# Kernel tuning notes

Hardware: AMD Instinct MI355X
Metric: run time of the kernel (lower is better)

Reference implementation:

```python
import jax, jax.numpy as jnp
import numpy as np

N, E, D, HID, OUT, R = 100000, 640000, 128, 128, 128, 8


def setup_inputs() -> dict:
    key = jax.random.key(0)
    ks = jax.random.split(key, 12)
    x = jax.random.normal(ks[0], (N, D), dtype=jnp.float32)
    src = jax.random.randint(ks[1], (E,), 0, N)
    dst = jax.random.randint(ks[2], (E,), 0, N)
    etype = jax.random.randint(ks[3], (E,), 0, R)
    s = 0.05
    W_rel = jax.random.normal(ks[4], (R, D, OUT), dtype=jnp.float32) * s
    loop_w = jax.random.normal(ks[5], (D, OUT), dtype=jnp.float32) * s
    rel_bias = jax.random.normal(ks[6], (OUT,), dtype=jnp.float32) * s
    W1 = jax.random.normal(ks[7], (D + HID, 2 * HID), dtype=jnp.float32) * s
    b1 = jax.random.normal(ks[8], (2 * HID,), dtype=jnp.float32) * s
    W2 = jax.random.normal(ks[9], (D + 2 * HID, OUT), dtype=jnp.float32) * s
    b2 = jax.random.normal(ks[10], (OUT,), dtype=jnp.float32) * s
    return {"x": x, "src": src, "dst": dst, "etype": etype,
            "W_rel": W_rel, "loop_w": loop_w, "rel_bias": rel_bias,
            "W1": W1, "b1": b1, "W2": W2, "b2": b2}


def reference(x, src, dst, etype, W_rel, loop_w, rel_bias, W1, b1, W2, b2):
    n = x.shape[0]
    # RelGraphConv (low_mem): transform all nodes once per relation, then
    # gather the (relation, src)-specific message per edge.  [R, N, OUT]
    h_rel = jnp.einsum('nd,rdo->rno', x, W_rel)
    m = h_rel[etype, src]                                   # [E, OUT]
    agg = jax.ops.segment_sum(m, dst, num_segments=n)       # sum at dst
    msg = agg + x @ loop_w + rel_bias                       # self-loop + bias
    # concat-MLP update (is_block=False -> dst_x = x), activation = tanh
    mid = jnp.tanh(jnp.concatenate([x, msg], axis=1) @ W1 + b1)
    return jnp.concatenate([x, mid], axis=1) @ W2 + b2
```

## Files before the change

### kernel.cpp

```cpp
#include <hip/hip_runtime.h>

#define NN 100000
#define NE 640000
#define RR 8
#define NBIN 800000

typedef unsigned short u16;
typedef u16 u16x4 __attribute__((ext_vector_type(4)));
typedef u16 u16x8 __attribute__((ext_vector_type(8)));
typedef __bf16 bf16x8 __attribute__((ext_vector_type(8)));
typedef float f32x4 __attribute__((ext_vector_type(4)));

#define OFF_MSG     0u
#define OFF_MIDB    51200000u
#define OFF_XB      102400000u
#define OFF_WT      128000000u
#define OFF_W1T     128296960u
#define OFF_W2T     128428032u
#define OFF_BUCKET  128527360u
#define OFF_CSROFF  131088384u
#define OFF_CUR     134289408u
#define OFF_PSUM    137490432u

__device__ inline u16 f2bf(float f) {
  unsigned u = __float_as_uint(f);
  u += 0x7FFF + ((u >> 16) & 1);
  return (u16)(u >> 16);
}
__device__ inline float bf2f(u16 h) { return __uint_as_float(((unsigned)h) << 16); }

__global__ void k_cvt_x(const float* __restrict__ x, u16* __restrict__ xb) {
  const int i = (blockIdx.x * 256 + threadIdx.x) * 4;
  const float4 v = *(const float4*)(x + i);
  u16x4 o;
  o.x = f2bf(v.x); o.y = f2bf(v.y); o.z = f2bf(v.z); o.w = f2bf(v.w);
  *(u16x4*)(xb + i) = o;
}

__global__ void k_cvt_wrel(const float* __restrict__ W, const float* __restrict__ Lw,
                           u16* __restrict__ Wt) {
  const int idx = blockIdx.x * 256 + threadIdx.x;
  const int r = idx >> 14, o = (idx >> 7) & 127, d = idx & 127;
  Wt[idx] = f2bf(r < 8 ? W[(r << 14) + (d << 7) + o] : Lw[(d << 7) + o]);
}

__global__ void k_cvt_w1(const float* __restrict__ W1, u16* __restrict__ W1t) {
  const int idx = blockIdx.x * 256 + threadIdx.x;
  const int o = idx >> 8, i = idx & 255;
  W1t[idx] = f2bf(W1[i * 256 + o]);
}

__global__ void k_cvt_w2(const float* __restrict__ W2, u16* __restrict__ W2t) {
  const int idx = blockIdx.x * 256 + threadIdx.x;
  const int o = idx / 384, i = idx % 384;
  W2t[idx] = f2bf(W2[i * 128 + o]);
}

__global__ void k_hist(const int* __restrict__ dst, const int* __restrict__ et,
                       int* __restrict__ cnt) {
  const int e = blockIdx.x * 256 + threadIdx.x;
  if (e < NE) atomicAdd(&cnt[dst[e] * 8 + et[e]], 1);
}

__global__ void k_scanA(const int* __restrict__ cnt, int* __restrict__ psum) {
  __shared__ int sc[256];
  const int tid = threadIdx.x, base = blockIdx.x * 1024 + tid * 4;
  int s = 0;
#pragma unroll
  for (int t = 0; t < 4; ++t) { const int i = base + t; if (i < NBIN) s += cnt[i]; }
  sc[tid] = s; __syncthreads();
  for (int d = 128; d > 0; d >>= 1) {
    if (tid < d) sc[tid] += sc[tid + d];
    __syncthreads();
  }
  if (tid == 0) psum[blockIdx.x] = sc[0];
}

__global__ void k_scanB(int* __restrict__ psum) {
  __shared__ int sc[1024];
  const int tid = threadIdx.x;
  const int v = (tid < 782) ? psum[tid] : 0;
  sc[tid] = v; __syncthreads();
  for (int d = 1; d < 1024; d <<= 1) {
    const int t = (tid >= d) ? sc[tid - d] : 0;
    __syncthreads();
    sc[tid] += t;
    __syncthreads();
  }
  if (tid < 782) psum[tid] = sc[tid] - v;
}

__global__ void k_scanC(int* __restrict__ cnt , const int* __restrict__ psum,
                        int* __restrict__ off) {
  __shared__ int sc[256];
  const int tid = threadIdx.x, base = blockIdx.x * 1024 + tid * 4;
  int c[4], s = 0;
#pragma unroll
  for (int t = 0; t < 4; ++t) {
    const int i = base + t;
    c[t] = (i < NBIN) ? cnt[i] : 0;
    s += c[t];
  }
  sc[tid] = s; __syncthreads();
  for (int d = 1; d < 256; d <<= 1) {
    const int t = (tid >= d) ? sc[tid - d] : 0;
    __syncthreads();
    sc[tid] += t;
    __syncthreads();
  }
  int run = psum[blockIdx.x] + sc[tid] - s;
#pragma unroll
  for (int t = 0; t < 4; ++t) {
    const int i = base + t;
    if (i < NBIN) { off[i] = run; cnt[i] = run; run += c[t]; }
  }
  if (blockIdx.x == 0 && tid == 0) off[NBIN] = NE;
}

__global__ void k_scatter(const int* __restrict__ src, const int* __restrict__ dst,
                          const int* __restrict__ et, int* __restrict__ cur,
                          int* __restrict__ bucket) {
  const int e = blockIdx.x * 256 + threadIdx.x;
  if (e < NE) {
    const int pos = atomicAdd(&cur[dst[e] * 8 + et[e]], 1);
    bucket[pos] = src[e];
  }
}

#define ATS 136
__global__ __launch_bounds__(256) void k_edge_msg(
    const u16* __restrict__ xb, const u16* __restrict__ Wt,
    const int* __restrict__ csroff, const int* __restrict__ bucket,
    const float* __restrict__ rel_bias, float* __restrict__ msg) {
  __shared__ u16 At[32 * ATS];
  __shared__ int soff[257];
  const int tid = threadIdx.x;
  const int v0 = blockIdx.x * 32;

  soff[tid] = csroff[v0 * 8 + tid];
  if (tid == 0) soff[256] = csroff[v0 * 8 + 256];

  const int wave = tid >> 6, lane = tid & 63;
  const int l16 = lane & 15, quad = lane >> 4;
  const int rt = wave & 1, cb = (wave >> 1) << 6;
  const int si = tid >> 3, sj = tid & 7;
  __syncthreads();

  f32x4 acc[4] = {};

  for (int r = 0; r < 9; ++r) {
    float a[16] = {};
    int pbeg, pend;
    if (r < 8) { pbeg = soff[si * 8 + r]; pend = soff[si * 8 + r + 1]; }
    else       { pbeg = 0; pend = 1; }
    for (int p = pbeg; p < pend; ++p) {
      const int s = (r < 8) ? bucket[p] : (v0 + si);
      const u16* xp = xb + ((size_t)s << 7) + sj * 16;
      const u16x8 h0 = *(const u16x8*)(xp);
      const u16x8 h1 = *(const u16x8*)(xp + 8);
#pragma unroll
      for (int t = 0; t < 8; ++t) { a[t] += bf2f(h0[t]); a[8 + t] += bf2f(h1[t]); }
    }
    u16x8 o0, o1;
#pragma unroll
    for (int t = 0; t < 8; ++t) { o0[t] = f2bf(a[t]); o1[t] = f2bf(a[8 + t]); }
    *(u16x8*)&At[si * ATS + sj * 16]     = o0;
    *(u16x8*)&At[si * ATS + sj * 16 + 8] = o1;
    __syncthreads();

    bf16x8 afr[4];
#pragma unroll
    for (int t = 0; t < 4; ++t)
      afr[t] = *(const bf16x8*)&At[(rt * 16 + l16) * ATS + quad * 8 + t * 32];
    const u16* wb = Wt + (r << 14);
#pragma unroll
    for (int c = 0; c < 4; ++c) {
      const u16* wp = wb + (size_t)(cb + c * 16 + l16) * 128 + quad * 8;
#pragma unroll
      for (int t = 0; t < 4; ++t)
        acc[c] = __builtin_amdgcn_mfma_f32_16x16x32_bf16(afr[t], *(const bf16x8*)(wp + t * 32), acc[c], 0, 0, 0);
    }
    __syncthreads();
  }

#pragma unroll
  for (int c = 0; c < 4; ++c) {
    const int col = cb + c * 16 + l16;
    const float bias = rel_bias[col];
#pragma unroll
    for (int reg = 0; reg < 4; ++reg) {
      const int row = v0 + rt * 16 + quad * 4 + reg;
      msg[(size_t)row * 128 + col] = acc[c][reg] + bias;
    }
  }
}

#define A1S 264
__global__ __launch_bounds__(256) void k_mlp1(
    const u16* __restrict__ xb, const float* __restrict__ msg,
    const u16* __restrict__ W1t, const float* __restrict__ b1,
    u16* __restrict__ midb) {
  __shared__ u16 At[32 * A1S];
  const int tid = threadIdx.x;
  const int v0 = blockIdx.x * 32;
  const int si = tid >> 3, sj = tid & 7;

  {
    const u16* xp = xb + ((size_t)(v0 + si) << 7) + sj * 16;
    *(u16x8*)&At[si * A1S + sj * 16]     = *(const u16x8*)(xp);
    *(u16x8*)&At[si * A1S + sj * 16 + 8] = *(const u16x8*)(xp + 8);
  }
  {
    const float* mp = msg + (size_t)(v0 + si) * 128 + sj * 16;
    u16x8 o0, o1;
#pragma unroll
    for (int t = 0; t < 8; ++t) { o0[t] = f2bf(mp[t]); o1[t] = f2bf(mp[8 + t]); }
    *(u16x8*)&At[si * A1S + 128 + sj * 16]     = o0;
    *(u16x8*)&At[si * A1S + 128 + sj * 16 + 8] = o1;
  }
  __syncthreads();

  const int wave = tid >> 6, lane = tid & 63;
  const int l16 = lane & 15, quad = lane >> 4;
  const int rt = wave & 1, ch = (wave >> 1) << 7;

  f32x4 acc[8] = {};
  for (int kt = 0; kt < 8; ++kt) {
    const bf16x8 af = *(const bf16x8*)&At[(rt * 16 + l16) * A1S + kt * 32 + quad * 8];
#pragma unroll
    for (int ct = 0; ct < 8; ++ct) {
      const u16* wp = W1t + (size_t)(ch + ct * 16 + l16) * 256 + kt * 32 + quad * 8;
      acc[ct] = __builtin_amdgcn_mfma_f32_16x16x32_bf16(af, *(const bf16x8*)(wp), acc[ct], 0, 0, 0);
    }
  }

#pragma unroll
  for (int ct = 0; ct < 8; ++ct) {
    const int col = ch + ct * 16 + l16;
    const float bias = b1[col];
#pragma unroll
    for (int reg = 0; reg < 4; ++reg) {
      const int row = v0 + rt * 16 + quad * 4 + reg;
      midb[(size_t)row * 256 + col] = f2bf(tanhf(acc[ct][reg] + bias));
    }
  }
}

#define A2S 392
__global__ __launch_bounds__(256) void k_mlp2(
    const u16* __restrict__ xb, const u16* __restrict__ midb,
    const u16* __restrict__ W2t, const float* __restrict__ b2,
    float* __restrict__ out) {
  __shared__ u16 At[32 * A2S];
  const int tid = threadIdx.x;
  const int v0 = blockIdx.x * 32;
  const int si = tid >> 3, sj = tid & 7;

  {
    const u16* xp = xb + ((size_t)(v0 + si) << 7) + sj * 16;
    *(u16x8*)&At[si * A2S + sj * 16]     = *(const u16x8*)(xp);
    *(u16x8*)&At[si * A2S + sj * 16 + 8] = *(const u16x8*)(xp + 8);
  }
  {
    const u16* mp = midb + ((size_t)(v0 + si) << 8) + sj * 32;
#pragma unroll
    for (int t = 0; t < 4; ++t)
      *(u16x8*)&At[si * A2S + 128 + sj * 32 + t * 8] = *(const u16x8*)(mp + t * 8);
  }
  __syncthreads();

  const int wave = tid >> 6, lane = tid & 63;
  const int l16 = lane & 15, quad = lane >> 4;
  const int rt = wave & 1, cb = (wave >> 1) << 6;

  f32x4 acc[4] = {};
  for (int kt = 0; kt < 12; ++kt) {
    const bf16x8 af = *(const bf16x8*)&At[(rt * 16 + l16) * A2S + kt * 32 + quad * 8];
#pragma unroll
    for (int ct = 0; ct < 4; ++ct) {
      const u16* wp = W2t + (size_t)(cb + ct * 16 + l16) * 384 + kt * 32 + quad * 8;
      acc[ct] = __builtin_amdgcn_mfma_f32_16x16x32_bf16(af, *(const bf16x8*)(wp), acc[ct], 0, 0, 0);
    }
  }

#pragma unroll
  for (int ct = 0; ct < 4; ++ct) {
    const int col = cb + ct * 16 + l16;
    const float bias = b2[col];
#pragma unroll
    for (int reg = 0; reg < 4; ++reg) {
      const int row = v0 + rt * 16 + quad * 4 + reg;
      out[(size_t)row * 128 + col] = acc[ct][reg] + bias;
    }
  }
}

extern "C" void kernel_launch(void* const* d_in, const int* in_sizes, int n_in,
                              void* d_out, int out_size, void* d_ws, size_t ws_size,
                              hipStream_t stream) {
  (void)in_sizes; (void)n_in; (void)out_size; (void)ws_size;
  const float* x        = (const float*)d_in[0];
  const int*   src      = (const int*)d_in[1];
  const int*   dst      = (const int*)d_in[2];
  const int*   et       = (const int*)d_in[3];
  const float* W_rel    = (const float*)d_in[4];
  const float* loop_w   = (const float*)d_in[5];
  const float* rel_bias = (const float*)d_in[6];
  const float* W1       = (const float*)d_in[7];
  const float* b1       = (const float*)d_in[8];
  const float* W2       = (const float*)d_in[9];
  const float* b2       = (const float*)d_in[10];
  float* out = (float*)d_out;

  char* ws = (char*)d_ws;
  float* msg    = (float*)(ws + OFF_MSG);
  u16*   midb   = (u16*)(ws + OFF_MIDB);
  u16*   xb     = (u16*)(ws + OFF_XB);
  u16*   Wt     = (u16*)(ws + OFF_WT);
  u16*   W1t    = (u16*)(ws + OFF_W1T);
  u16*   W2t    = (u16*)(ws + OFF_W2T);
  int*   bucket = (int*)(ws + OFF_BUCKET);
  int*   csroff = (int*)(ws + OFF_CSROFF);
  int*   cur    = (int*)(ws + OFF_CUR);
  int*   psum   = (int*)(ws + OFF_PSUM);

  hipMemsetAsync(cur, 0, (size_t)NBIN * 4, stream);

  k_cvt_x   <<<(NN * 128) / 1024, 256, 0, stream>>>(x, xb);
  k_cvt_wrel<<<(9 * 16384) / 256, 256, 0, stream>>>(W_rel, loop_w, Wt);
  k_cvt_w1  <<<(256 * 256) / 256, 256, 0, stream>>>(W1, W1t);
  k_cvt_w2  <<<(128 * 384) / 256, 256, 0, stream>>>(W2, W2t);

  k_hist    <<<(NE + 255) / 256, 256, 0, stream>>>(dst, et, cur);
  k_scanA   <<<782, 256, 0, stream>>>(cur, psum);
  k_scanB   <<<1, 1024, 0, stream>>>(psum);
  k_scanC   <<<782, 256, 0, stream>>>(cur, psum, csroff);
  k_scatter <<<(NE + 255) / 256, 256, 0, stream>>>(src, dst, et, cur, bucket);

  k_edge_msg<<<NN / 32, 256, 0, stream>>>(xb, Wt, csroff, bucket, rel_bias, msg);
  k_mlp1    <<<NN / 32, 256, 0, stream>>>(xb, msg, W1t, b1, midb);
  k_mlp2    <<<NN / 32, 256, 0, stream>>>(xb, midb, W2t, b2, out);
}
```

Baseline: 638.7 us.

## Rebalance edge aggregation with flat edge-parallel LDS atomics over relation-grouped bins

```diff
diff --git a/kernel.cpp b/kernel.cpp
--- a/kernel.cpp
+++ b/kernel.cpp
@@ -29,6 +29,10 @@
 }
 __device__ inline float bf2f(u16 h) { return __uint_as_float(((unsigned)h) << 16); }
 
+__device__ inline int edge_bin(int d, int r) {
+  return (((d >> 5) * 2 + (r >> 2)) << 7) + ((d & 31) << 2) + (r & 3);
+}
+
 __global__ void k_cvt_x(const float* __restrict__ x, u16* __restrict__ xb) {
   const int i = (blockIdx.x * 256 + threadIdx.x) * 4;
   const float4 v = *(const float4*)(x + i);
@@ -59,7 +63,7 @@
 __global__ void k_hist(const int* __restrict__ dst, const int* __restrict__ et,
                        int* __restrict__ cnt) {
   const int e = blockIdx.x * 256 + threadIdx.x;
-  if (e < NE) atomicAdd(&cnt[dst[e] * 8 + et[e]], 1);
+  if (e < NE) atomicAdd(&cnt[edge_bin(dst[e], et[e])], 1);
 }
 
 __global__ void k_scanA(const int* __restrict__ cnt, int* __restrict__ psum) {
@@ -119,66 +123,93 @@
 
 __global__ void k_scatter(const int* __restrict__ src, const int* __restrict__ dst,
                           const int* __restrict__ et, int* __restrict__ cur,
-                          int* __restrict__ bucket) {
+                          unsigned* __restrict__ bucket) {
   const int e = blockIdx.x * 256 + threadIdx.x;
   if (e < NE) {
-    const int pos = atomicAdd(&cur[dst[e] * 8 + et[e]], 1);
-    bucket[pos] = src[e];
-  }
-}
-
-#define ATS 136
+    const int d = dst[e], r = et[e];
+    const int pos = atomicAdd(&cur[edge_bin(d, r)], 1);
+    bucket[pos] = (unsigned)src[e] | ((unsigned)(d & 31) << 17) | ((unsigned)(r & 3) << 22);
+  }
+}
+
+#define ACCS 132
 __global__ __launch_bounds__(256) void k_edge_msg(
     const u16* __restrict__ xb, const u16* __restrict__ Wt,
-    const int* __restrict__ csroff, const int* __restrict__ bucket,
+    const int* __restrict__ csroff, const unsigned* __restrict__ bucket,
     const float* __restrict__ rel_bias, float* __restrict__ msg) {
-  __shared__ u16 At[32 * ATS];
-  __shared__ int soff[257];
+  __shared__ float accF[4 * 32 * ACCS];
   const int tid = threadIdx.x;
   const int v0 = blockIdx.x * 32;
-
-  soff[tid] = csroff[v0 * 8 + tid];
-  if (tid == 0) soff[256] = csroff[v0 * 8 + 256];
-
   const int wave = tid >> 6, lane = tid & 63;
   const int l16 = lane & 15, quad = lane >> 4;
   const int rt = wave & 1, cb = (wave >> 1) << 6;
-  const int si = tid >> 3, sj = tid & 7;
-  __syncthreads();
+
+  const int base0 = csroff[blockIdx.x * 256];
+  const int base1 = csroff[blockIdx.x * 256 + 128];
+  const int base2 = csroff[blockIdx.x * 256 + 256];
 
   f32x4 acc[4] = {};
 
-  for (int r = 0; r < 9; ++r) {
-    float a[16] = {};
-    int pbeg, pend;
-    if (r < 8) { pbeg = soff[si * 8 + r]; pend = soff[si * 8 + r + 1]; }
-    else       { pbeg = 0; pend = 1; }
-    for (int p = pbeg; p < pend; ++p) {
-      const int s = (r < 8) ? bucket[p] : (v0 + si);
-      const u16* xp = xb + ((size_t)s << 7) + sj * 16;
+  {
+    const u16* xp = xb + ((size_t)(v0 + rt * 16 + l16) << 7) + quad * 8;
+    bf16x8 afr[4];
+#pragma unroll
+    for (int t = 0; t < 4; ++t) afr[t] = *(const bf16x8*)(xp + t * 32);
+    const u16* wb = Wt + (8 << 14);
+#pragma unroll
+    for (int c = 0; c < 4; ++c) {
+      const u16* wp = wb + (size_t)(cb + c * 16 + l16) * 128 + quad * 8;
+#pragma unroll
+      for (int t = 0; t < 4; ++t)
+        acc[c] = __builtin_amdgcn_mfma_f32_16x16x32_bf16(afr[t], *(const bf16x8*)(wp + t * 32), acc[c], 0, 0, 0);
+    }
+  }
+
+#pragma unroll
+  for (int ph = 0; ph < 2; ++ph) {
+    for (int i = tid; i < 4 * 32 * ACCS / 4; i += 256)
+      *(f32x4*)&accF[i * 4] = (f32x4){0.f, 0.f, 0.f, 0.f};
+    __syncthreads();
+
+    const int pstart = ph ? base1 : base0;
+    const int nt = ((ph ? base2 : base1) - pstart) * 8;
+    for (int t = tid; t < nt; t += 256) {
+      const unsigned w = bucket[pstart + (t >> 3)];
+      const int sj = t & 7;
+      const u16* xp = xb + ((size_t)(w & 131071u) << 7) + sj * 16;
       const u16x8 h0 = *(const u16x8*)(xp);
       const u16x8 h1 = *(const u16x8*)(xp + 8);
-#pragma unroll
-      for (int t = 0; t < 8; ++t) { a[t] += bf2f(h0[t]); a[8 + t] += bf2f(h1[t]); }
-    }
-    u16x8 o0, o1;
-#pragma unroll
-    for (int t = 0; t < 8; ++t) { o0[t] = f2bf(a[t]); o1[t] = f2bf(a[8 + t]); }
-    *(u16x8*)&At[si * ATS + sj * 16]     = o0;
-    *(u16x8*)&At[si * ATS + sj * 16 + 8] = o1;
-    __syncthreads();
-
-    bf16x8 afr[4];
-#pragma unroll
-    for (int t = 0; t < 4; ++t)
-      afr[t] = *(const bf16x8*)&At[(rt * 16 + l16) * ATS + quad * 8 + t * 32];
-    const u16* wb = Wt + (r << 14);
-#pragma unroll
-    for (int c = 0; c < 4; ++c) {
-      const u16* wp = wb + (size_t)(cb + c * 16 + l16) * 128 + quad * 8;
-#pragma unroll
-      for (int t = 0; t < 4; ++t)
-        acc[c] = __builtin_amdgcn_mfma_f32_16x16x32_bf16(afr[t], *(const bf16x8*)(wp + t * 32), acc[c], 0, 0, 0);
+      float* ac = accF + ((w >> 22) & 3u) * (32 * ACCS) + ((w >> 17) & 31u) * ACCS + sj * 16;
+#pragma unroll
+      for (int i = 0; i < 8; ++i) {
+        atomicAdd(ac + i,     bf2f(h0[i]));
+        atomicAdd(ac + 8 + i, bf2f(h1[i]));
+      }
+    }
+    __syncthreads();
+
+#pragma unroll
+    for (int q = 0; q < 4; ++q) {
+      const int r = ph * 4 + q;
+      bf16x8 afr[4];
+#pragma unroll
+      for (int t = 0; t < 4; ++t) {
+        const int off = q * (32 * ACCS) + (rt * 16 + l16) * ACCS + quad * 8 + t * 32;
+        const f32x4 a0 = *(const f32x4*)&accF[off];
+        const f32x4 a1 = *(const f32x4*)&accF[off + 4];
+        union { u16x8 u; bf16x8 b; } cv;
+        cv.u[0] = f2bf(a0[0]); cv.u[1] = f2bf(a0[1]); cv.u[2] = f2bf(a0[2]); cv.u[3] = f2bf(a0[3]);
+        cv.u[4] = f2bf(a1[0]); cv.u[5] = f2bf(a1[1]); cv.u[6] = f2bf(a1[2]); cv.u[7] = f2bf(a1[3]);
+        afr[t] = cv.b;
+      }
+      const u16* wb = Wt + (r << 14);
+#pragma unroll
+      for (int c = 0; c < 4; ++c) {
+        const u16* wp = wb + (size_t)(cb + c * 16 + l16) * 128 + quad * 8;
+#pragma unroll
+        for (int t = 0; t < 4; ++t)
+          acc[c] = __builtin_amdgcn_mfma_f32_16x16x32_bf16(afr[t], *(const bf16x8*)(wp + t * 32), acc[c], 0, 0, 0);
+      }
     }
     __syncthreads();
   }
@@ -313,16 +344,16 @@
   float* out = (float*)d_out;
 
   char* ws = (char*)d_ws;
-  float* msg    = (float*)(ws + OFF_MSG);
-  u16*   midb   = (u16*)(ws + OFF_MIDB);
-  u16*   xb     = (u16*)(ws + OFF_XB);
-  u16*   Wt     = (u16*)(ws + OFF_WT);
-  u16*   W1t    = (u16*)(ws + OFF_W1T);
-  u16*   W2t    = (u16*)(ws + OFF_W2T);
-  int*   bucket = (int*)(ws + OFF_BUCKET);
-  int*   csroff = (int*)(ws + OFF_CSROFF);
-  int*   cur    = (int*)(ws + OFF_CUR);
-  int*   psum   = (int*)(ws + OFF_PSUM);
+  float*    msg    = (float*)(ws + OFF_MSG);
+  u16*      midb   = (u16*)(ws + OFF_MIDB);
+  u16*      xb     = (u16*)(ws + OFF_XB);
+  u16*      Wt     = (u16*)(ws + OFF_WT);
+  u16*      W1t    = (u16*)(ws + OFF_W1T);
+  u16*      W2t    = (u16*)(ws + OFF_W2T);
+  unsigned* bucket = (unsigned*)(ws + OFF_BUCKET);
+  int*      csroff = (int*)(ws + OFF_CSROFF);
+  int*      cur    = (int*)(ws + OFF_CUR);
+  int*      psum   = (int*)(ws + OFF_PSUM);
 
   hipMemsetAsync(cur, 0, (size_t)NBIN * 4, stream);
 
```

After: 975.7 us. +52.8%, slower.
